# Kernel tuning notes

Measured on AMD Instinct MI355X. Metric: run time of the kernel, lower is better.

The kernel has to match this reference:

```python
import jax, jax.numpy as jnp
import numpy as np

HEADS = 8
C_OUT = 256


def _gconv1x1(x, w, g):
    # x: (B, Cin, H, W); w: (Cout, Cin//g) -> grouped 1x1 conv, out (B, g, Cout//g, L)
    B, C, H, W = x.shape
    xr = x.reshape(B, g, C // g, H * W)
    wr = w.reshape(g, w.shape[0] // g, C // g)
    return jnp.einsum('god,bgdl->bgol', wr, xr)


def _sine_pe(d, L, dtype):
    # standard transformer sinusoidal PE laid out as (channels=d, positions=L)
    pos = jnp.arange(L, dtype=jnp.float32)
    i = jnp.arange(0, d, 2, dtype=jnp.float32)
    inv_freq = jnp.exp(-np.float32(np.log(10000.0)) * i / d)  # (d/2,)
    ang = inv_freq[:, None] * pos[None, :]                    # (d/2, L)
    pe = jnp.zeros((d, L), jnp.float32)
    pe = pe.at[0::2].set(jnp.sin(ang)).at[1::2].set(jnp.cos(ang))
    return pe.astype(dtype)


def setup_inputs() -> dict:
    key = jax.random.key(0)
    k1, k2, k3, k4 = jax.random.split(key, 4)
    B, Cin, H, W = 2, 256, 24, 24
    std = np.float32(np.sqrt(2.0 / C_OUT))  # kaiming_normal fan_out, relu gain
    x = jax.random.normal(k1, (B, Cin, H, W), jnp.float32)
    wq = jax.random.normal(k2, (C_OUT, Cin // HEADS), jnp.float32) * std
    wk = jax.random.normal(k3, (C_OUT, Cin // HEADS), jnp.float32) * std
    wv = jax.random.normal(k4, (C_OUT, Cin // HEADS), jnp.float32) * std
    return {"x": x, "wq": wq, "wk": wk, "wv": wv}


def reference(x, wq, wk, wv):
    B, Cin, H, W = x.shape
    g = HEADS
    d = C_OUT // g
    L = H * W
    q = _gconv1x1(x, wq, g)  # (B, g, d, L)
    k = _gconv1x1(x, wk, g)
    v = _gconv1x1(x, wv, g)
    # sinusoidal positional encoding added to keys over flattened spatial dim
    pe = _sine_pe(C_OUT, L, x.dtype)
    k = (k.reshape(B, C_OUT, L) + pe[None]).reshape(B, g, d, L)
    # NOTE: original torch code flattens batch AND heads into the attention dim
    qf = q.transpose(0, 1, 3, 2).reshape(-1, d)   # (N, d), N = B*g*L
    kf = k.transpose(2, 0, 1, 3).reshape(d, -1)   # (d, N)
    vf = v.transpose(0, 1, 3, 2).reshape(-1, d)   # (N, d)
    scale = np.float32(np.sqrt(g / C_OUT))        # = 1/sqrt(d)
    att = jax.nn.softmax(qf @ kf * scale, axis=-1)  # (N, N)
    out = att @ vf                                  # (N, d)
    out = out.reshape(B, g, L, d).transpose(0, 1, 3, 2).reshape(B, C_OUT, H, W)
    return out
```

## Files before the change

### kernel.cpp

```cpp
#include <hip/hip_runtime.h>


#define LSP   576
#define NROW  9216
#define DH    32
#define NW    8
#define KPW   (NROW / NW)
#define BN    32
#define NTILE (KPW / BN)
#define VSTR  40
#define PSTR  40
#define QB    36
#define SZ    ((size_t)NROW * DH)
#define SZP   (SZ + 2048)

typedef __attribute__((ext_vector_type(8))) short bh8;
typedef __attribute__((ext_vector_type(4))) float f4;

static __device__ __forceinline__ float bf2f(unsigned short u) {
    union { unsigned int i; float f; } w; w.i = (unsigned int)u << 16; return w.f;
}
static __device__ __forceinline__ unsigned short f2bf(float x) {
    union { float f; unsigned int i; } w; w.f = x;
    unsigned int u = w.i;
    return (unsigned short)((u + 0x7fffu + ((u >> 16) & 1u)) >> 16);
}
static __device__ __forceinline__ unsigned int pkbf(float a, float b) {
    return (unsigned int)f2bf(a) | ((unsigned int)f2bf(b) << 16);
}

#define MFMA(a, b, c) __builtin_amdgcn_mfma_f32_16x16x32_bf16(a, b, c, 0, 0, 0)

__global__ __launch_bounds__(256) void sa_proj_kernel(
    const float* __restrict__ x,
    const float* __restrict__ wq, const float* __restrict__ wk, const float* __restrict__ wv,
    unsigned short* __restrict__ Qhi, unsigned short* __restrict__ Qlo,
    unsigned short* __restrict__ Khi, unsigned short* __restrict__ Vt)
{
    __shared__ __align__(16) float xs[32 * 40];
    __shared__ float vt[32 * 37];
    __shared__ float wqs[32 * 33], wks[32 * 33], wvs[32 * 33];
    const int t = threadIdx.x;
    const int bg = blockIdx.x >> 4;
    const int part = blockIdx.x & 15;
    const int g = bg & 7;
    const int l0 = part * 36;

    const float* xp = x + (size_t)bg * 32 * LSP + l0;
    for (int i = t; i < 32 * 9; i += 256) {
        int d = i / 9, seg = i % 9;
        *(float4*)(xs + d * 40 + seg * 4) = *(const float4*)(xp + d * LSP + seg * 4);
    }
    for (int i = t; i < 1024; i += 256) {
        int o = i >> 5, d = i & 31;
        wqs[o * 33 + d] = wq[(g * 32 + o) * 32 + d];
        wks[o * 33 + d] = wk[(g * 32 + o) * 32 + d];
        wvs[o * 33 + d] = wv[(g * 32 + o) * 32 + d];
    }
    __syncthreads();

    const float scale = 0.17677669529663687f;
    for (int idx = t; idx < 32 * 36; idx += 256) {
        const int o = idx & 31;
        const int lloc = idx >> 5;
        const int l = l0 + lloc;
        float aq = 0.f, ak = 0.f, av = 0.f;
        #pragma unroll
        for (int d = 0; d < 32; d++) {
            const float xv = xs[d * 40 + lloc];
            aq = fmaf(wqs[o * 33 + d], xv, aq);
            ak = fmaf(wks[o * 33 + d], xv, ak);
            av = fmaf(wvs[o * 33 + d], xv, av);
        }
        aq *= scale;
        const int c = g * 32 + o;
        const float i2 = (float)(c & ~1);
        const float inv = __expf(-0.035977892078031968f * i2);
        float sv, cv;
        __sincosf(inv * (float)l, &sv, &cv);
        ak += (c & 1) ? cv : sv;

        const size_t row = (size_t)bg * LSP + l;
        const unsigned short h = f2bf(aq);
        Qhi[row * 32 + o] = h;
        Qlo[row * 32 + o] = f2bf(aq - bf2f(h));
        Khi[row * 32 + o] = f2bf(ak);
        vt[o * 37 + lloc] = av;
    }
    __syncthreads();

    for (int idx = t; idx < 32 * 36; idx += 256) {
        const int d = idx / 36;
        const int cc = idx - d * 36;
        const int n = bg * LSP + l0 + cc;
        Vt[(size_t)(n >> 5) * 1024 + d * 32 + (n & 31)] = f2bf(vt[d * 37 + cc]);
    }
}

__global__ __launch_bounds__(512, 2) void sa_attn_kernel(
    const unsigned short* __restrict__ Qhi, const unsigned short* __restrict__ Qlo,
    const unsigned short* __restrict__ Khi, const unsigned short* __restrict__ Vt,
    float* __restrict__ out)
{
    __shared__ __align__(16) unsigned short shm[NW * 3200];
    const int t = threadIdx.x;
    const int wave = t >> 6, lane = t & 63;
    const int quad = lane >> 4, l16 = lane & 15;
    const int n0 = blockIdx.x * QB;

    unsigned short* vs = shm + wave * 3200;
    unsigned short* ps = vs + 32 * VSTR;

    const bh8 qh0 = *(const bh8*)(Qhi + (size_t)(n0 + l16) * DH + quad * 8);
    const bh8 ql0 = *(const bh8*)(Qlo + (size_t)(n0 + l16) * DH + quad * 8);
    const bh8 qh1 = *(const bh8*)(Qhi + (size_t)(n0 + 16 + l16) * DH + quad * 8);
    const bh8 ql1 = *(const bh8*)(Qlo + (size_t)(n0 + 16 + l16) * DH + quad * 8);
    const bh8 qh2 = *(const bh8*)(Qhi + (size_t)(n0 + 32 + l16) * DH + quad * 8);
    const bh8 ql2 = *(const bh8*)(Qlo + (size_t)(n0 + 32 + l16) * DH + quad * 8);

    f4 o00 = {0.f,0.f,0.f,0.f}, o01 = {0.f,0.f,0.f,0.f};
    f4 o10 = {0.f,0.f,0.f,0.f}, o11 = {0.f,0.f,0.f,0.f};
    f4 o20 = {0.f,0.f,0.f,0.f}, o21 = {0.f,0.f,0.f,0.f};
    float ls0 = 0.f, ls1 = 0.f, ls2 = 0.f;
    const f4 zf = {0.f,0.f,0.f,0.f};

    const int kbase = wave * KPW;
    bh8 kf0 = *(const bh8*)(Khi + (size_t)(kbase + l16) * DH + quad * 8);
    bh8 kf1 = *(const bh8*)(Khi + (size_t)(kbase + 16 + l16) * DH + quad * 8);
    uint4 va = *(const uint4*)(Vt + (size_t)(kbase >> 5) * 1024 + lane * 8);
    uint4 vb = *(const uint4*)(Vt + (size_t)(kbase >> 5) * 1024 + 512 + lane * 8);

    for (int tile = 0; tile < NTILE; ++tile) {
        *(uint4*)(vs + (lane >> 2) * VSTR + (lane & 3) * 8) = va;
        *(uint4*)(vs + (16 + (lane >> 2)) * VSTR + (lane & 3) * 8) = vb;

        f4 s00 = MFMA(kf0, ql0, zf); s00 = MFMA(kf0, qh0, s00);
        f4 s01 = MFMA(kf0, ql1, zf); s01 = MFMA(kf0, qh1, s01);
        f4 s02 = MFMA(kf0, ql2, zf); s02 = MFMA(kf0, qh2, s02);
        f4 s10 = MFMA(kf1, ql0, zf); s10 = MFMA(kf1, qh0, s10);
        f4 s11 = MFMA(kf1, ql1, zf); s11 = MFMA(kf1, qh1, s11);
        f4 s12 = MFMA(kf1, ql2, zf); s12 = MFMA(kf1, qh2, s12);

        if (tile + 1 < NTILE) {
            const int kn = kbase + (tile + 1) * BN;
            kf0 = *(const bh8*)(Khi + (size_t)(kn + l16) * DH + quad * 8);
            kf1 = *(const bh8*)(Khi + (size_t)(kn + 16 + l16) * DH + quad * 8);
            va = *(const uint4*)(Vt + (size_t)(kn >> 5) * 1024 + lane * 8);
            vb = *(const uint4*)(Vt + (size_t)(kn >> 5) * 1024 + 512 + lane * 8);
        }

        #define EXPST(S, GRP, JJ, LSV)                                        \
        {                                                                     \
            const float e0 = __expf(S[0]), e1 = __expf(S[1]);                 \
            const float e2 = __expf(S[2]), e3 = __expf(S[3]);                 \
            LSV += (e0 + e1) + (e2 + e3);                                     \
            uint2 pk; pk.x = pkbf(e0, e1); pk.y = pkbf(e2, e3);               \
            *(uint2*)(ps + (GRP * 16 + l16) * PSTR + JJ * 16 + quad * 4) = pk;\
        }
        EXPST(s00, 0, 0, ls0) EXPST(s01, 1, 0, ls1) EXPST(s02, 2, 0, ls2)
        EXPST(s10, 0, 1, ls0) EXPST(s11, 1, 1, ls1) EXPST(s12, 2, 1, ls2)
        #undef EXPST

        const bh8 pa0 = *(const bh8*)(ps + l16 * PSTR + quad * 8);
        const bh8 pa1 = *(const bh8*)(ps + (16 + l16) * PSTR + quad * 8);
        const bh8 pa2 = *(const bh8*)(ps + (32 + l16) * PSTR + quad * 8);
        const bh8 v0  = *(const bh8*)(vs + l16 * VSTR + quad * 8);
        const bh8 v1  = *(const bh8*)(vs + (16 + l16) * VSTR + quad * 8);
        o00 = MFMA(pa0, v0, o00); o01 = MFMA(pa0, v1, o01);
        o10 = MFMA(pa1, v0, o10); o11 = MFMA(pa1, v1, o11);
        o20 = MFMA(pa2, v0, o20); o21 = MFMA(pa2, v1, o21);
    }

    ls0 += __shfl_xor(ls0, 16); ls0 += __shfl_xor(ls0, 32);
    ls1 += __shfl_xor(ls1, 16); ls1 += __shfl_xor(ls1, 32);
    ls2 += __shfl_xor(ls2, 16); ls2 += __shfl_xor(ls2, 32);

    __syncthreads();
    float* mo = (float*)shm;
    float* mls = mo + NW * 1160;
    float* mp = mo + wave * 1160;
    #pragma unroll
    for (int reg = 0; reg < 4; ++reg) {
        const int q0 = quad * 4 + reg;
        mp[l16 * 36 + q0]             = o00[reg];
        mp[(16 + l16) * 36 + q0]      = o01[reg];
        mp[l16 * 36 + 16 + q0]        = o10[reg];
        mp[(16 + l16) * 36 + 16 + q0] = o11[reg];
        if (quad == 0) {
            mp[l16 * 36 + 32 + reg]        = o20[reg];
            mp[(16 + l16) * 36 + 32 + reg] = o21[reg];
        }
    }
    if (quad == 0) {
        mls[wave * 36 + l16]      = ls0;
        mls[wave * 36 + 16 + l16] = ls1;
        if (l16 < 4) mls[wave * 36 + 32 + l16] = ls2;
    }
    __syncthreads();

    const int bg = n0 / LSP;
    const int l0 = n0 - bg * LSP;
    for (int c = t; c < 32 * QB; c += 512) {
        const int d = c / QB;
        const int q = c - d * QB;
        float num = 0.f, den = 0.f;
        #pragma unroll
        for (int w2 = 0; w2 < NW; ++w2) {
            num += mo[w2 * 1160 + c];
            den += mls[w2 * 36 + q];
        }
        out[((size_t)(bg * 32 + d)) * LSP + l0 + q] = num / den;
    }
}

extern "C" void kernel_launch(void* const* d_in, const int* in_sizes, int n_in,
                              void* d_out, int out_size, void* d_ws, size_t ws_size,
                              hipStream_t stream) {
    (void)in_sizes; (void)n_in; (void)out_size; (void)ws_size;
    const float* x  = (const float*)d_in[0];
    const float* wq = (const float*)d_in[1];
    const float* wk = (const float*)d_in[2];
    const float* wv = (const float*)d_in[3];

    unsigned short* ws = (unsigned short*)d_ws;
    unsigned short* Qhi = ws;
    unsigned short* Qlo = ws + SZP;
    unsigned short* Khi = ws + 2 * SZP;
    unsigned short* Vt  = ws + 3 * SZP;
    float* out = (float*)d_out;

    sa_proj_kernel<<<256, 256, 0, stream>>>(x, wq, wk, wv, Qhi, Qlo, Khi, Vt);
    sa_attn_kernel<<<256, 512, 0, stream>>>(Qhi, Qlo, Khi, Vt, out);
}
```

Baseline: 102.2 us.

## Load V fragments directly to registers, double-buffer P, compute row sums via MFMA

Permutes the V layout written by the projection kernel so the attention kernel can load V MFMA operands straight from global memory into registers, dropping the per-tile LDS staging of V. P tiles are double-buffered in LDS and the P·V MFMAs are software-pipelined one tile behind the QK^T/exp stage. The softmax denominators are now accumulated with an extra MFMA against a ones vector instead of scalar adds and cross-lane shuffles, and bf16 packing uses the HIP paired conversion intrinsic. This adds MFMA work and reshapes the merge buffers in exchange for fewer LDS writes and VALU ops per tile. Because the denominators now sum bf16-rounded probabilities rather than fp32 values, results may differ slightly from before.

```diff
diff --git a/kernel.cpp b/kernel.cpp
--- a/kernel.cpp
+++ b/kernel.cpp
@@ -1,4 +1,5 @@
 #include <hip/hip_runtime.h>
+#include <hip/hip_bf16.h>
 
 
 #define LSP   576
@@ -8,7 +9,6 @@
 #define KPW   (NROW / NW)
 #define BN    32
 #define NTILE (KPW / BN)
-#define VSTR  40
 #define PSTR  40
 #define QB    36
 #define SZ    ((size_t)NROW * DH)
@@ -26,7 +26,9 @@
     return (unsigned short)((u + 0x7fffu + ((u >> 16) & 1u)) >> 16);
 }
 static __device__ __forceinline__ unsigned int pkbf(float a, float b) {
-    return (unsigned int)f2bf(a) | ((unsigned int)f2bf(b) << 16);
+    union { __hip_bfloat162 h2; unsigned int u; } w;
+    w.h2 = __float22bfloat162_rn(make_float2(a, b));
+    return w.u;
 }
 
 #define MFMA(a, b, c) __builtin_amdgcn_mfma_f32_16x16x32_bf16(a, b, c, 0, 0, 0)
@@ -93,7 +95,10 @@
         const int d = idx / 36;
         const int cc = idx - d * 36;
         const int n = bg * LSP + l0 + cc;
-        Vt[(size_t)(n >> 5) * 1024 + d * 32 + (n & 31)] = f2bf(vt[d * 37 + cc]);
+        const int k = n & 31;
+        const int cperm = (k < 16) ? ((k >> 2) * 8 + (k & 3))
+                                   : (((k - 16) >> 2) * 8 + ((k - 16) & 3) + 4);
+        Vt[(size_t)(n >> 5) * 1024 + d * 32 + cperm] = f2bf(vt[d * 37 + cc]);
     }
 }
 
@@ -102,14 +107,14 @@
     const unsigned short* __restrict__ Khi, const unsigned short* __restrict__ Vt,
     float* __restrict__ out)
 {
-    __shared__ __align__(16) unsigned short shm[NW * 3200];
+    __shared__ __align__(16) unsigned short shm[NW * 2 * 48 * PSTR];
     const int t = threadIdx.x;
     const int wave = t >> 6, lane = t & 63;
     const int quad = lane >> 4, l16 = lane & 15;
     const int n0 = blockIdx.x * QB;
 
-    unsigned short* vs = shm + wave * 3200;
-    unsigned short* ps = vs + 32 * VSTR;
+    unsigned short* psA = shm + wave * 2 * 48 * PSTR;
+    unsigned short* psB = psA + 48 * PSTR;
 
     const bh8 qh0 = *(const bh8*)(Qhi + (size_t)(n0 + l16) * DH + quad * 8);
     const bh8 ql0 = *(const bh8*)(Qlo + (size_t)(n0 + l16) * DH + quad * 8);
@@ -118,22 +123,25 @@
     const bh8 qh2 = *(const bh8*)(Qhi + (size_t)(n0 + 32 + l16) * DH + quad * 8);
     const bh8 ql2 = *(const bh8*)(Qlo + (size_t)(n0 + 32 + l16) * DH + quad * 8);
 
+    const short oneb = (short)0x3F80;
+    const bh8 ones = {oneb, oneb, oneb, oneb, oneb, oneb, oneb, oneb};
+
     f4 o00 = {0.f,0.f,0.f,0.f}, o01 = {0.f,0.f,0.f,0.f};
     f4 o10 = {0.f,0.f,0.f,0.f}, o11 = {0.f,0.f,0.f,0.f};
     f4 o20 = {0.f,0.f,0.f,0.f}, o21 = {0.f,0.f,0.f,0.f};
-    float ls0 = 0.f, ls1 = 0.f, ls2 = 0.f;
+    f4 lo0 = {0.f,0.f,0.f,0.f}, lo1 = {0.f,0.f,0.f,0.f}, lo2 = {0.f,0.f,0.f,0.f};
     const f4 zf = {0.f,0.f,0.f,0.f};
 
     const int kbase = wave * KPW;
+    const int tile0 = kbase >> 5;
+
     bh8 kf0 = *(const bh8*)(Khi + (size_t)(kbase + l16) * DH + quad * 8);
     bh8 kf1 = *(const bh8*)(Khi + (size_t)(kbase + 16 + l16) * DH + quad * 8);
-    uint4 va = *(const uint4*)(Vt + (size_t)(kbase >> 5) * 1024 + lane * 8);
-    uint4 vb = *(const uint4*)(Vt + (size_t)(kbase >> 5) * 1024 + 512 + lane * 8);
+    bh8 vf0 = *(const bh8*)(Vt + (size_t)tile0 * 1024 + l16 * 32 + quad * 8);
+    bh8 vf1 = *(const bh8*)(Vt + (size_t)tile0 * 1024 + (16 + l16) * 32 + quad * 8);
+    bh8 pv0 = vf0, pv1 = vf1;
 
     for (int tile = 0; tile < NTILE; ++tile) {
-        *(uint4*)(vs + (lane >> 2) * VSTR + (lane & 3) * 8) = va;
-        *(uint4*)(vs + (16 + (lane >> 2)) * VSTR + (lane & 3) * 8) = vb;
-
         f4 s00 = MFMA(kf0, ql0, zf); s00 = MFMA(kf0, qh0, s00);
         f4 s01 = MFMA(kf0, ql1, zf); s01 = MFMA(kf0, qh1, s01);
         f4 s02 = MFMA(kf0, ql2, zf); s02 = MFMA(kf0, qh2, s02);
@@ -141,60 +149,79 @@
         f4 s11 = MFMA(kf1, ql1, zf); s11 = MFMA(kf1, qh1, s11);
         f4 s12 = MFMA(kf1, ql2, zf); s12 = MFMA(kf1, qh2, s12);
 
-        if (tile + 1 < NTILE) {
-            const int kn = kbase + (tile + 1) * BN;
-            kf0 = *(const bh8*)(Khi + (size_t)(kn + l16) * DH + quad * 8);
-            kf1 = *(const bh8*)(Khi + (size_t)(kn + 16 + l16) * DH + quad * 8);
-            va = *(const uint4*)(Vt + (size_t)(kn >> 5) * 1024 + lane * 8);
-            vb = *(const uint4*)(Vt + (size_t)(kn >> 5) * 1024 + 512 + lane * 8);
-        }
-
-        #define EXPST(S, GRP, JJ, LSV)                                        \
-        {                                                                     \
-            const float e0 = __expf(S[0]), e1 = __expf(S[1]);                 \
-            const float e2 = __expf(S[2]), e3 = __expf(S[3]);                 \
-            LSV += (e0 + e1) + (e2 + e3);                                     \
-            uint2 pk; pk.x = pkbf(e0, e1); pk.y = pkbf(e2, e3);               \
-            *(uint2*)(ps + (GRP * 16 + l16) * PSTR + JJ * 16 + quad * 4) = pk;\
-        }
-        EXPST(s00, 0, 0, ls0) EXPST(s01, 1, 0, ls1) EXPST(s02, 2, 0, ls2)
-        EXPST(s10, 0, 1, ls0) EXPST(s11, 1, 1, ls1) EXPST(s12, 2, 1, ls2)
-        #undef EXPST
-
-        const bh8 pa0 = *(const bh8*)(ps + l16 * PSTR + quad * 8);
-        const bh8 pa1 = *(const bh8*)(ps + (16 + l16) * PSTR + quad * 8);
-        const bh8 pa2 = *(const bh8*)(ps + (32 + l16) * PSTR + quad * 8);
-        const bh8 v0  = *(const bh8*)(vs + l16 * VSTR + quad * 8);
-        const bh8 v1  = *(const bh8*)(vs + (16 + l16) * VSTR + quad * 8);
-        o00 = MFMA(pa0, v0, o00); o01 = MFMA(pa0, v1, o01);
-        o10 = MFMA(pa1, v0, o10); o11 = MFMA(pa1, v1, o11);
-        o20 = MFMA(pa2, v0, o20); o21 = MFMA(pa2, v1, o21);
-    }
-
-    ls0 += __shfl_xor(ls0, 16); ls0 += __shfl_xor(ls0, 32);
-    ls1 += __shfl_xor(ls1, 16); ls1 += __shfl_xor(ls1, 32);
-    ls2 += __shfl_xor(ls2, 16); ls2 += __shfl_xor(ls2, 32);
+        const int tn = (tile + 1 < NTILE) ? tile + 1 : tile;
+        const int kn = kbase + tn * BN;
+        kf0 = *(const bh8*)(Khi + (size_t)(kn + l16) * DH + quad * 8);
+        kf1 = *(const bh8*)(Khi + (size_t)(kn + 16 + l16) * DH + quad * 8);
+
+        unsigned short* pc = (tile & 1) ? psB : psA;
+        uint4 w0, w1, w2;
+        w0.x = pkbf(__expf(s00[0]), __expf(s00[1]));
+        w0.y = pkbf(__expf(s00[2]), __expf(s00[3]));
+        w0.z = pkbf(__expf(s10[0]), __expf(s10[1]));
+        w0.w = pkbf(__expf(s10[2]), __expf(s10[3]));
+        *(uint4*)(pc + l16 * PSTR + quad * 8) = w0;
+        w1.x = pkbf(__expf(s01[0]), __expf(s01[1]));
+        w1.y = pkbf(__expf(s01[2]), __expf(s01[3]));
+        w1.z = pkbf(__expf(s11[0]), __expf(s11[1]));
+        w1.w = pkbf(__expf(s11[2]), __expf(s11[3]));
+        *(uint4*)(pc + (16 + l16) * PSTR + quad * 8) = w1;
+        w2.x = pkbf(__expf(s02[0]), __expf(s02[1]));
+        w2.y = pkbf(__expf(s02[2]), __expf(s02[3]));
+        w2.z = pkbf(__expf(s12[0]), __expf(s12[1]));
+        w2.w = pkbf(__expf(s12[2]), __expf(s12[3]));
+        *(uint4*)(pc + (32 + l16) * PSTR + quad * 8) = w2;
+
+        if (tile > 0) {
+            const unsigned short* pp = (tile & 1) ? psA : psB;
+            const bh8 pa0 = *(const bh8*)(pp + l16 * PSTR + quad * 8);
+            const bh8 pa1 = *(const bh8*)(pp + (16 + l16) * PSTR + quad * 8);
+            const bh8 pa2 = *(const bh8*)(pp + (32 + l16) * PSTR + quad * 8);
+            o00 = MFMA(pa0, pv0, o00); o01 = MFMA(pa0, pv1, o01);
+            o10 = MFMA(pa1, pv0, o10); o11 = MFMA(pa1, pv1, o11);
+            o20 = MFMA(pa2, pv0, o20); o21 = MFMA(pa2, pv1, o21);
+            lo0 = MFMA(pa0, ones, lo0);
+            lo1 = MFMA(pa1, ones, lo1);
+            lo2 = MFMA(pa2, ones, lo2);
+        }
+        pv0 = vf0; pv1 = vf1;
+        vf0 = *(const bh8*)(Vt + (size_t)(tile0 + tn) * 1024 + l16 * 32 + quad * 8);
+        vf1 = *(const bh8*)(Vt + (size_t)(tile0 + tn) * 1024 + (16 + l16) * 32 + quad * 8);
+    }
+    {
+        const unsigned short* pp = (NTILE & 1) ? psA : psB;
+        const bh8 pa0 = *(const bh8*)(pp + l16 * PSTR + quad * 8);
+        const bh8 pa1 = *(const bh8*)(pp + (16 + l16) * PSTR + quad * 8);
+        const bh8 pa2 = *(const bh8*)(pp + (32 + l16) * PSTR + quad * 8);
+        o00 = MFMA(pa0, pv0, o00); o01 = MFMA(pa0, pv1, o01);
+        o10 = MFMA(pa1, pv0, o10); o11 = MFMA(pa1, pv1, o11);
+        o20 = MFMA(pa2, pv0, o20); o21 = MFMA(pa2, pv1, o21);
+        lo0 = MFMA(pa0, ones, lo0);
+        lo1 = MFMA(pa1, ones, lo1);
+        lo2 = MFMA(pa2, ones, lo2);
+    }
 
     __syncthreads();
     float* mo = (float*)shm;
-    float* mls = mo + NW * 1160;
-    float* mp = mo + wave * 1160;
+    float* mls = mo + NW * 1536;
+    float* mp = mo + wave * 1536;
     #pragma unroll
     for (int reg = 0; reg < 4; ++reg) {
         const int q0 = quad * 4 + reg;
-        mp[l16 * 36 + q0]             = o00[reg];
-        mp[(16 + l16) * 36 + q0]      = o01[reg];
-        mp[l16 * 36 + 16 + q0]        = o10[reg];
-        mp[(16 + l16) * 36 + 16 + q0] = o11[reg];
-        if (quad == 0) {
-            mp[l16 * 36 + 32 + reg]        = o20[reg];
-            mp[(16 + l16) * 36 + 32 + reg] = o21[reg];
-        }
-    }
-    if (quad == 0) {
-        mls[wave * 36 + l16]      = ls0;
-        mls[wave * 36 + 16 + l16] = ls1;
-        if (l16 < 4) mls[wave * 36 + 32 + l16] = ls2;
+        mp[l16 * 48 + q0]             = o00[reg];
+        mp[(16 + l16) * 48 + q0]      = o01[reg];
+        mp[l16 * 48 + 16 + q0]        = o10[reg];
+        mp[(16 + l16) * 48 + 16 + q0] = o11[reg];
+        mp[l16 * 48 + 32 + q0]        = o20[reg];
+        mp[(16 + l16) * 48 + 32 + q0] = o21[reg];
+    }
+    if (l16 == 0) {
+        #pragma unroll
+        for (int reg = 0; reg < 4; ++reg) {
+            mls[wave * 48 + quad * 4 + reg]      = lo0[reg];
+            mls[wave * 48 + 16 + quad * 4 + reg] = lo1[reg];
+            mls[wave * 48 + 32 + quad * 4 + reg] = lo2[reg];
+        }
     }
     __syncthreads();
 
@@ -206,8 +233,8 @@
         float num = 0.f, den = 0.f;
         #pragma unroll
         for (int w2 = 0; w2 < NW; ++w2) {
-            num += mo[w2 * 1160 + c];
-            den += mls[w2 * 36 + q];
+            num += mo[w2 * 1536 + d * 48 + q];
+            den += mls[w2 * 48 + q];
         }
         out[((size_t)(bg * 32 + d)) * LSP + l0 + q] = num / den;
     }
```

Result: faster. 98.84 us (-3.2%).
